# Kernel tuning notes

Hardware: AMD Instinct MI355X
Metric: run time of the kernel (lower is better)

The kernel has to match this reference:

```python
import jax, jax.numpy as jnp
import numpy as np

D = 1024; NH = 16; HD = D // NH; B = 2; L = 2048
BASE_FAST = (1.0 + 5.0 ** 0.5) / 2.0
BASE_SLOW = 1618.0
BASE_GLU = 16180.0
ALPHA_ATTN = 0.42; ALPHA_MLP = 1.07; ALPHA_ADV = 1.0
H_GATE = max(8, D // 4)   # rope_gate hidden
H_NU = max(4, D // 8)     # DuplexViscosity hidden
LN_EPS = 1e-5


def _rope_cos_sin(seq_len, dim, base, dtype=jnp.float32):
    idx = jnp.arange(0, dim, 2, dtype=dtype) / float(dim)
    inv = 1.0 / (base ** idx)
    t = jnp.arange(seq_len, dtype=dtype)
    freqs = jnp.outer(t, inv)                       # (L, D/2)
    emb = jnp.concatenate([freqs, freqs], axis=-1)  # (L, D)
    return jnp.cos(emb)[None], jnp.sin(emb)[None]   # (1, L, D)


def _rotate_half(x):
    x1, x2 = jnp.split(x, 2, axis=-1)
    return jnp.concatenate([-x2, x1], axis=-1)


def _apply_rope(x, cos, sin):
    return x * cos + _rotate_half(x) * sin


def setup_inputs() -> dict:
    key = jax.random.key(0)
    ks = jax.random.split(key, 16)
    std = 0.02
    # all Linear weights stored as (in, out) so forward is x @ W + b
    return {
        "z": jax.random.normal(ks[0], (B, L, D), jnp.float32),
        "Wq": jax.random.normal(ks[1], (D, D), jnp.float32) * std,
        "bq": jnp.zeros((D,), jnp.float32),
        "Wk": jax.random.normal(ks[2], (D, D), jnp.float32) * std,
        "bk": jnp.zeros((D,), jnp.float32),
        "Wv": jax.random.normal(ks[3], (D, D), jnp.float32) * std,
        "bv": jnp.zeros((D,), jnp.float32),
        "Wcoh": jax.random.normal(ks[4], (D, D), jnp.float32) * std,
        "gamma": jnp.zeros((1,), jnp.float32),
        "rg_w1": jax.random.normal(ks[5], (D, H_GATE), jnp.float32) * std,
        "rg_b1": jnp.zeros((H_GATE,), jnp.float32),
        "rg_w2": jax.random.normal(ks[6], (H_GATE, 1), jnp.float32) * std,
        "rg_b2": jnp.zeros((1,), jnp.float32),
        "nu_diff": jnp.asarray(0.2, jnp.float32),
        "nu_adv": jnp.asarray(0.01, jnp.float32),
        "nu_w1": jax.random.normal(ks[7], (D, H_NU), jnp.float32) * std,
        "nu_b1": jnp.zeros((H_NU,), jnp.float32),
        "nu_w2": jax.random.normal(ks[8], (H_NU, 1), jnp.float32) * std,
        "nu_b2": jnp.zeros((1,), jnp.float32),
        "Wu": jax.random.normal(ks[9], (D, D), jnp.float32) * std,
        "bu": jnp.zeros((D,), jnp.float32),
        "Wg": jax.random.normal(ks[10], (D, D), jnp.float32) * std,
        "bg": jnp.zeros((D,), jnp.float32),
        "ln_w": jnp.ones((D,), jnp.float32),
        "ln_b": jnp.zeros((D,), jnp.float32),
        "Cw": jax.random.normal(ks[11], (D, D), jnp.float32) * std,
        "Cb": jnp.zeros((D,), jnp.float32),
    }


def reference(z, Wq, bq, Wk, bk, Wv, bv, Wcoh, gamma, rg_w1, rg_b1, rg_w2, rg_b2,
              nu_diff, nu_adv, nu_w1, nu_b1, nu_w2, nu_b2, Wu, bu, Wg, bg,
              ln_w, ln_b, Cw, Cb):
    b, l, d = z.shape
    dt = z.dtype
    # causal cumulative mean pool[t] = mean(z[0..t])
    pool = jnp.cumsum(z, axis=1) / jnp.arange(1, l + 1, dtype=dt)[None, :, None]

    # QKV projections
    Q = z @ Wq + bq
    K_raw = z @ Wk + bk
    V = z @ Wv + bv

    # global coherence bias: (B, Lq, Lk)
    gk = pool @ Wcoh
    gb = jnp.einsum('bld,bmd->blm', gk, K_raw) * (d ** -0.5)
    gb = jnp.tanh(gamma[0]) * gb

    # hybrid RoPE gate (small MLP on pool, exact gelu as in torch)
    gate = jax.nn.sigmoid(jax.nn.gelu(pool @ rg_w1 + rg_b1, approximate=False) @ rg_w2 + rg_b2)  # (B,L,1)
    cos_f, sin_f = _rope_cos_sin(l, d, BASE_FAST, dt)
    cos_s, sin_s = _rope_cos_sin(l, d, BASE_SLOW, dt)
    cos = gate * cos_f + (1.0 - gate) * cos_s
    sin = gate * sin_f + (1.0 - gate) * sin_s
    Qr = _apply_rope(Q, cos, sin)
    Kr = _apply_rope(K_raw, cos, sin)

    # multi-head causal attention with fused coherence bias
    Qh = Qr.reshape(b, l, NH, HD).transpose(0, 2, 1, 3)
    Kh = Kr.reshape(b, l, NH, HD).transpose(0, 2, 1, 3)
    Vh = V.reshape(b, l, NH, HD).transpose(0, 2, 1, 3)
    logits = jnp.einsum('bhld,bhmd->bhlm', Qh, Kh) * (HD ** -0.5)
    logits = logits + gb[:, None]
    causal = jnp.tril(jnp.ones((l, l), bool))
    logits = jnp.where(causal[None, None], logits, -jnp.inf)
    attn = jax.nn.softmax(logits, axis=-1)
    attn_out = jnp.einsum('bhlm,bhmd->bhld', attn, Vh).transpose(0, 2, 1, 3).reshape(b, l, d)
    attn_w = attn.mean(axis=1)

    # DuplexViscosity on causal pool
    delta = jnp.tanh(jnp.tanh(pool @ nu_w1 + nu_b1) @ nu_w2 + nu_b2) * jnp.abs(nu_adv)
    nu_b = jnp.abs(nu_diff) + delta  # (B,L,1)

    # GLU branch with fixed slow-base RoPE
    cos_g, sin_g = _rope_cos_sin(l, d, BASE_GLU, dt)
    z_glu = _apply_rope(z, cos_g, sin_g)
    bilinear = (z_glu @ Wu + bu) * (z_glu @ Wg + bg)
    adv = -(ALPHA_ADV * nu_b) * bilinear
    mu = adv.mean(axis=-1, keepdims=True)
    var = ((adv - mu) ** 2).mean(axis=-1, keepdims=True)
    adv_n = (adv - mu) * jax.lax.rsqrt(var + LN_EPS) * ln_w + ln_b
    mlp_out = adv_n @ Cw + Cb

    z_next = z + ALPHA_ATTN * attn_out + ALPHA_MLP * mlp_out
    return z_next, attn_w
```

## Files before the change

kernel.cpp:

```cpp
#include <hip/hip_runtime.h>

#define DD 1024
#define NHH 16
#define HDD 64
#define BB 2
#define LL 2048
#define MM (BB*LL)
#define HG 256
#define HN 128

#define LOG_FAST 0.48121182f
#define LOG_SLOW 7.3889461f
#define LOG_GLU  9.6915312f
#define SCL 0.18033688f

typedef __attribute__((ext_vector_type(8))) short short8;
typedef __attribute__((ext_vector_type(4))) float f32x4;

__device__ __forceinline__ float gelu_f(float x) {
    return 0.5f * x * (1.0f + erff(x * 0.70710678f));
}

__device__ __forceinline__ ushort f2b(float x) {
    unsigned u = __float_as_uint(x);
    unsigned r = (u + 0x7FFFu + ((u >> 16) & 1u)) >> 16;
    return (ushort)r;
}

__device__ __forceinline__ float b2f(ushort x) {
    return __uint_as_float(((unsigned)x) << 16);
}

__device__ __forceinline__ void gl_lds16(const ushort* g, ushort* l) {
    __builtin_amdgcn_global_load_lds(
        (const __attribute__((address_space(1))) unsigned int*)g,
        (__attribute__((address_space(3))) unsigned int*)l, 16, 0, 0);
}

#define SWZC(row, c8) (((((row) << 3) | ((c8) ^ ((row) & 7)))) << 3)

__device__ __forceinline__ void stage_tile(const ushort* gsrc, int rstride,
                                           ushort* lds, int tid) {
    int wid = tid >> 6;
#pragma unroll
    for (int r = 0; r < 2; ++r) {
        int c = r * 256 + tid;
        int row = c >> 3;
        int c8 = (c & 7) ^ (row & 7);
        gl_lds16(gsrc + (size_t)row * rstride + c8 * 8,
                 lds + (size_t)(r * 256 + wid * 64) * 8);
    }
}

#define LCH 128
#define NCH 16
__global__ void pool_scan1(const float* __restrict__ z, float* __restrict__ part,
                           float* __restrict__ ctot, ushort* __restrict__ zb) {
    int ch = blockIdx.x, dg = blockIdx.y, b = blockIdx.z;
    int d = dg * 256 + threadIdx.x;
    size_t base = ((size_t)b * LL + ch * LCH) * DD + d;
    const float* zp = z + base;
    float* pp = part + base;
    ushort* zo = zb + base;
    float s = 0.f;
    for (int t = 0; t < LCH; ++t) {
        float v = zp[(size_t)t * DD];
        s += v;
        pp[(size_t)t * DD] = s;
        zo[(size_t)t * DD] = f2b(v);
    }
    ctot[((size_t)b * NCH + ch) * DD + d] = s;
}
__global__ void pool_scan2(const float* __restrict__ part, const float* __restrict__ ctot,
                           ushort* __restrict__ poolb) {
    int ch = blockIdx.x, dg = blockIdx.y, b = blockIdx.z;
    int d = dg * 256 + threadIdx.x;
    float off = 0.f;
    for (int c = 0; c < ch; ++c) off += ctot[((size_t)b * NCH + c) * DD + d];
    int t0 = ch * LCH;
    size_t base = ((size_t)b * LL + t0) * DD + d;
    const float* pp = part + base;
    ushort* po = poolb + base;
    for (int t = 0; t < LCH; ++t) {
        po[(size_t)t * DD] = f2b((pp[(size_t)t * DD] + off) / (float)(t0 + t + 1));
    }
}

__global__ void f2bT4_kernel(const float* __restrict__ W0, const float* __restrict__ W1,
                             const float* __restrict__ W2, const float* __restrict__ W3,
                             ushort* __restrict__ Wt) {
    const float* W = blockIdx.z == 0 ? W0 : (blockIdx.z == 1 ? W1 :
                     (blockIdx.z == 2 ? W2 : W3));
    ushort* dst = Wt + (size_t)blockIdx.z * 1024 * 1024;
    __shared__ float t[32][33];
    int n0 = blockIdx.x * 32, k0 = blockIdx.y * 32;
    int tx = threadIdx.x & 31, ty = threadIdx.x >> 5;
#pragma unroll
    for (int j = 0; j < 4; ++j)
        t[ty + j * 8][tx] = W[(size_t)(k0 + ty + j * 8) * 1024 + n0 + tx];
    __syncthreads();
#pragma unroll
    for (int j = 0; j < 4; ++j)
        dst[(size_t)(n0 + ty + j * 8) * 1024 + k0 + tx] = f2b(t[tx][ty + j * 8]);
}

__global__ void f2bT_rgnu(const float* __restrict__ Wrg, const float* __restrict__ Wnu,
                          ushort* __restrict__ WtRG, ushort* __restrict__ WtNU) {
    int zc = blockIdx.z;
    if (zc == 1 && blockIdx.x >= 4) return;
    const float* W = zc == 0 ? Wrg : Wnu;
    ushort* dst = zc == 0 ? WtRG : WtNU;
    int Ndim = zc == 0 ? HG : HN;
    __shared__ float t[32][33];
    int n0 = blockIdx.x * 32, k0 = blockIdx.y * 32;
    int tx = threadIdx.x & 31, ty = threadIdx.x >> 5;
#pragma unroll
    for (int j = 0; j < 4; ++j)
        t[ty + j * 8][tx] = W[(size_t)(k0 + ty + j * 8) * Ndim + n0 + tx];
    __syncthreads();
#pragma unroll
    for (int j = 0; j < 4; ++j)
        dst[(size_t)(n0 + ty + j * 8) * 1024 + k0 + tx] = f2b(t[tx][ty + j * 8]);
}

__global__ void f2bT3_kernel(const float* __restrict__ W0, const float* __restrict__ W1,
                             const float* __restrict__ W2, ushort* __restrict__ Wt) {
    const float* W = blockIdx.z == 0 ? W0 : (blockIdx.z == 1 ? W1 : W2);
    ushort* dst = Wt + (size_t)blockIdx.z * 1024 * 1024;
    __shared__ float t[32][33];
    int n0 = blockIdx.x * 32, k0 = blockIdx.y * 32;
    int tx = threadIdx.x & 31, ty = threadIdx.x >> 5;
#pragma unroll
    for (int j = 0; j < 4; ++j)
        t[ty + j * 8][tx] = W[(size_t)(k0 + ty + j * 8) * 1024 + n0 + tx];
    __syncthreads();
#pragma unroll
    for (int j = 0; j < 4; ++j)
        dst[(size_t)(n0 + ty + j * 8) * 1024 + k0 + tx] = f2b(t[tx][ty + j * 8]);
}

__global__ __launch_bounds__(256) void gemm_mfma(
        const ushort* __restrict__ A, const ushort* __restrict__ Wt,
        const float* __restrict__ bias, float* __restrict__ C, int Ndim) {
    __shared__ ushort As[4096];
    __shared__ ushort Bs[4096];
    int tid = threadIdx.x;
    int wid = tid >> 6, lane = tid & 63;
    int n0 = blockIdx.x * 128, m0 = blockIdx.y * 128;
    int wm = wid >> 1, wn = wid & 1;
    int quad = lane >> 4, l16 = lane & 15;

    f32x4 acc[4][4];
#pragma unroll
    for (int mi = 0; mi < 4; ++mi)
#pragma unroll
        for (int ni = 0; ni < 4; ++ni) acc[mi][ni] = (f32x4){0.f, 0.f, 0.f, 0.f};

    int c0 = wid * 128 + lane;
    int c1 = c0 + 64;
    const ushort* Ag0 = A + (size_t)(m0 + (c0 & 127)) * 1024 + (c0 >> 7) * 8;
    const ushort* Ag1 = A + (size_t)(m0 + (c1 & 127)) * 1024 + (c1 >> 7) * 8;
    const ushort* Bg0 = Wt + (size_t)(n0 + (c0 & 127)) * 1024 + (c0 >> 7) * 8;
    const ushort* Bg1 = Wt + (size_t)(n0 + (c1 & 127)) * 1024 + (c1 >> 7) * 8;
    ushort* Al0 = As + wid * 1024;
    ushort* Al1 = As + wid * 1024 + 512;
    ushort* Bl0 = Bs + wid * 1024;
    ushort* Bl1 = Bs + wid * 1024 + 512;

    const ushort* a_rd = &As[(quad * 128 + wm * 64 + l16) * 8];
    const ushort* b_rd = &Bs[(quad * 128 + wn * 64 + l16) * 8];

    for (int kb = 0; kb < 1024; kb += 32) {
        gl_lds16(Ag0 + kb, Al0);
        gl_lds16(Ag1 + kb, Al1);
        gl_lds16(Bg0 + kb, Bl0);
        gl_lds16(Bg1 + kb, Bl1);
        __syncthreads();
        short8 af[4], bf[4];
#pragma unroll
        for (int mi = 0; mi < 4; ++mi)
            af[mi] = *(const short8*)(a_rd + mi * 16 * 8);
#pragma unroll
        for (int ni = 0; ni < 4; ++ni)
            bf[ni] = *(const short8*)(b_rd + ni * 16 * 8);
#pragma unroll
        for (int mi = 0; mi < 4; ++mi)
#pragma unroll
            for (int ni = 0; ni < 4; ++ni)
                acc[mi][ni] = __builtin_amdgcn_mfma_f32_16x16x32_bf16(
                    af[mi], bf[ni], acc[mi][ni], 0, 0, 0);
        __syncthreads();
    }
    int bcol[4];
    float bval[4];
#pragma unroll
    for (int ni = 0; ni < 4; ++ni) {
        bcol[ni] = n0 + wn * 64 + ni * 16 + l16;
        bval[ni] = bias ? bias[bcol[ni]] : 0.f;
    }
#pragma unroll
    for (int mi = 0; mi < 4; ++mi) {
#pragma unroll
        for (int r = 0; r < 4; ++r) {
            int row = m0 + wm * 64 + mi * 16 + quad * 4 + r;
            float* Cp = C + (size_t)row * Ndim;
#pragma unroll
            for (int ni = 0; ni < 4; ++ni)
                Cp[bcol[ni]] = acc[mi][ni][r] + bval[ni];
        }
    }
}

__global__ __launch_bounds__(256) void gemm_mfma3(
        const ushort* __restrict__ A, const ushort* __restrict__ Wt,
        const float* __restrict__ b0, const float* __restrict__ b1,
        const float* __restrict__ b2, float* __restrict__ C,
        ushort* __restrict__ K16r) {
    int zid = blockIdx.z;
    const ushort* W = Wt + (size_t)zid * 1024 * 1024;
    const float* bias = zid == 0 ? b0 : (zid == 1 ? b1 : b2);
    float* Cz = C + (size_t)zid * (size_t)MM * DD;
    __shared__ ushort As[4096];
    __shared__ ushort Bs[4096];
    int tid = threadIdx.x;
    int wid = tid >> 6, lane = tid & 63;
    int n0 = blockIdx.x * 128, m0 = blockIdx.y * 128;
    int wm = wid >> 1, wn = wid & 1;
    int quad = lane >> 4, l16 = lane & 15;

    f32x4 acc[4][4];
#pragma unroll
    for (int mi = 0; mi < 4; ++mi)
#pragma unroll
        for (int ni = 0; ni < 4; ++ni) acc[mi][ni] = (f32x4){0.f, 0.f, 0.f, 0.f};

    int c0 = wid * 128 + lane;
    int c1 = c0 + 64;
    const ushort* Ag0 = A + (size_t)(m0 + (c0 & 127)) * 1024 + (c0 >> 7) * 8;
    const ushort* Ag1 = A + (size_t)(m0 + (c1 & 127)) * 1024 + (c1 >> 7) * 8;
    const ushort* Bg0 = W + (size_t)(n0 + (c0 & 127)) * 1024 + (c0 >> 7) * 8;
    const ushort* Bg1 = W + (size_t)(n0 + (c1 & 127)) * 1024 + (c1 >> 7) * 8;
    ushort* Al0 = As + wid * 1024;
    ushort* Al1 = As + wid * 1024 + 512;
    ushort* Bl0 = Bs + wid * 1024;
    ushort* Bl1 = Bs + wid * 1024 + 512;

    const ushort* a_rd = &As[(quad * 128 + wm * 64 + l16) * 8];
    const ushort* b_rd = &Bs[(quad * 128 + wn * 64 + l16) * 8];

    for (int kb = 0; kb < 1024; kb += 32) {
        gl_lds16(Ag0 + kb, Al0);
        gl_lds16(Ag1 + kb, Al1);
        gl_lds16(Bg0 + kb, Bl0);
        gl_lds16(Bg1 + kb, Bl1);
        __syncthreads();
        short8 af[4], bf[4];
#pragma unroll
        for (int mi = 0; mi < 4; ++mi)
            af[mi] = *(const short8*)(a_rd + mi * 16 * 8);
#pragma unroll
        for (int ni = 0; ni < 4; ++ni)
            bf[ni] = *(const short8*)(b_rd + ni * 16 * 8);
#pragma unroll
        for (int mi = 0; mi < 4; ++mi)
#pragma unroll
            for (int ni = 0; ni < 4; ++ni)
                acc[mi][ni] = __builtin_amdgcn_mfma_f32_16x16x32_bf16(
                    af[mi], bf[ni], acc[mi][ni], 0, 0, 0);
        __syncthreads();
    }
    float bval[4];
    int bcol[4];
#pragma unroll
    for (int ni = 0; ni < 4; ++ni) {
        bcol[ni] = n0 + wn * 64 + ni * 16 + l16;
        bval[ni] = bias[bcol[ni]];
    }
    bool doK = (zid == 1) && (K16r != nullptr);
#pragma unroll
    for (int mi = 0; mi < 4; ++mi) {
#pragma unroll
        for (int r = 0; r < 4; ++r) {
            int row = m0 + wm * 64 + mi * 16 + quad * 4 + r;
            float* Cp = Cz + (size_t)row * 1024;
            ushort* Kp = K16r + (size_t)row * 1024;
#pragma unroll
            for (int ni = 0; ni < 4; ++ni) {
                float v = acc[mi][ni][r] + bval[ni];
                Cp[bcol[ni]] = v;
                if (doK) Kp[bcol[ni]] = f2b(v);
            }
        }
    }
}

__global__ __launch_bounds__(256) void gemm_mfma_b16out(
        const ushort* __restrict__ A, const ushort* __restrict__ Wt,
        ushort* __restrict__ C, int Ndim) {
    __shared__ ushort As[4096];
    __shared__ ushort Bs[4096];
    int tid = threadIdx.x;
    int wid = tid >> 6, lane = tid & 63;
    int n0 = blockIdx.x * 128, m0 = blockIdx.y * 128;
    int wm = wid >> 1, wn = wid & 1;
    int quad = lane >> 4, l16 = lane & 15;

    f32x4 acc[4][4];
#pragma unroll
    for (int mi = 0; mi < 4; ++mi)
#pragma unroll
        for (int ni = 0; ni < 4; ++ni) acc[mi][ni] = (f32x4){0.f, 0.f, 0.f, 0.f};

    int c0 = wid * 128 + lane;
    int c1 = c0 + 64;
    const ushort* Ag0 = A + (size_t)(m0 + (c0 & 127)) * 1024 + (c0 >> 7) * 8;
    const ushort* Ag1 = A + (size_t)(m0 + (c1 & 127)) * 1024 + (c1 >> 7) * 8;
    const ushort* Bg0 = Wt + (size_t)(n0 + (c0 & 127)) * 1024 + (c0 >> 7) * 8;
    const ushort* Bg1 = Wt + (size_t)(n0 + (c1 & 127)) * 1024 + (c1 >> 7) * 8;
    ushort* Al0 = As + wid * 1024;
    ushort* Al1 = As + wid * 1024 + 512;
    ushort* Bl0 = Bs + wid * 1024;
    ushort* Bl1 = Bs + wid * 1024 + 512;

    const ushort* a_rd = &As[(quad * 128 + wm * 64 + l16) * 8];
    const ushort* b_rd = &Bs[(quad * 128 + wn * 64 + l16) * 8];

    for (int kb = 0; kb < 1024; kb += 32) {
        gl_lds16(Ag0 + kb, Al0);
        gl_lds16(Ag1 + kb, Al1);
        gl_lds16(Bg0 + kb, Bl0);
        gl_lds16(Bg1 + kb, Bl1);
        __syncthreads();
        short8 af[4], bf[4];
#pragma unroll
        for (int mi = 0; mi < 4; ++mi)
            af[mi] = *(const short8*)(a_rd + mi * 16 * 8);
#pragma unroll
        for (int ni = 0; ni < 4; ++ni)
            bf[ni] = *(const short8*)(b_rd + ni * 16 * 8);
#pragma unroll
        for (int mi = 0; mi < 4; ++mi)
#pragma unroll
            for (int ni = 0; ni < 4; ++ni)
                acc[mi][ni] = __builtin_amdgcn_mfma_f32_16x16x32_bf16(
                    af[mi], bf[ni], acc[mi][ni], 0, 0, 0);
        __syncthreads();
    }
#pragma unroll
    for (int mi = 0; mi < 4; ++mi) {
#pragma unroll
        for (int r = 0; r < 4; ++r) {
            int row = m0 + wm * 64 + mi * 16 + quad * 4 + r;
            ushort* Cp = C + (size_t)row * Ndim;
#pragma unroll
            for (int ni = 0; ni < 4; ++ni)
                Cp[n0 + wn * 64 + ni * 16 + l16] = f2b(acc[mi][ni][r]);
        }
    }
}

__global__ __launch_bounds__(256) void gemm_gates(
        const ushort* __restrict__ A, const ushort* __restrict__ WtRG,
        const ushort* __restrict__ WtNU, const float* __restrict__ rg_b1,
        const float* __restrict__ nu_b1, float* __restrict__ H1,
        float* __restrict__ N1) {
    int bx = blockIdx.x;
    bool isH = bx < 2;
    const ushort* Wt = isH ? WtRG : WtNU;
    const float* bias = isH ? rg_b1 : nu_b1;
    float* C = isH ? H1 : N1;
    int Ndim = isH ? HG : HN;
    int n0 = isH ? bx * 128 : 0;
    int m0 = blockIdx.y * 128;
    __shared__ ushort As[4096];
    __shared__ ushort Bs[4096];
    int tid = threadIdx.x;
    int wid = tid >> 6, lane = tid & 63;
    int wm = wid >> 1, wn = wid & 1;
    int quad = lane >> 4, l16 = lane & 15;

    f32x4 acc[4][4];
#pragma unroll
    for (int mi = 0; mi < 4; ++mi)
#pragma unroll
        for (int ni = 0; ni < 4; ++ni) acc[mi][ni] = (f32x4){0.f, 0.f, 0.f, 0.f};

    int c0 = wid * 128 + lane;
    int c1 = c0 + 64;
    const ushort* Ag0 = A + (size_t)(m0 + (c0 & 127)) * 1024 + (c0 >> 7) * 8;
    const ushort* Ag1 = A + (size_t)(m0 + (c1 & 127)) * 1024 + (c1 >> 7) * 8;
    const ushort* Bg0 = Wt + (size_t)(n0 + (c0 & 127)) * 1024 + (c0 >> 7) * 8;
    const ushort* Bg1 = Wt + (size_t)(n0 + (c1 & 127)) * 1024 + (c1 >> 7) * 8;
    ushort* Al0 = As + wid * 1024;
    ushort* Al1 = As + wid * 1024 + 512;
    ushort* Bl0 = Bs + wid * 1024;
    ushort* Bl1 = Bs + wid * 1024 + 512;

    const ushort* a_rd = &As[(quad * 128 + wm * 64 + l16) * 8];
    const ushort* b_rd = &Bs[(quad * 128 + wn * 64 + l16) * 8];

    for (int kb = 0; kb < 1024; kb += 32) {
        gl_lds16(Ag0 + kb, Al0);
        gl_lds16(Ag1 + kb, Al1);
        gl_lds16(Bg0 + kb, Bl0);
        gl_lds16(Bg1 + kb, Bl1);
        __syncthreads();
        short8 af[4], bf[4];
#pragma unroll
        for (int mi = 0; mi < 4; ++mi)
            af[mi] = *(const short8*)(a_rd + mi * 16 * 8);
#pragma unroll
        for (int ni = 0; ni < 4; ++ni)
            bf[ni] = *(const short8*)(b_rd + ni * 16 * 8);
#pragma unroll
        for (int mi = 0; mi < 4; ++mi)
#pragma unroll
            for (int ni = 0; ni < 4; ++ni)
                acc[mi][ni] = __builtin_amdgcn_mfma_f32_16x16x32_bf16(
                    af[mi], bf[ni], acc[mi][ni], 0, 0, 0);
        __syncthreads();
    }
    int bcol[4];
    float bval[4];
#pragma unroll
    for (int ni = 0; ni < 4; ++ni) {
        bcol[ni] = n0 + wn * 64 + ni * 16 + l16;
        bval[ni] = bias[bcol[ni]];
    }
#pragma unroll
    for (int mi = 0; mi < 4; ++mi) {
#pragma unroll
        for (int r = 0; r < 4; ++r) {
            int row = m0 + wm * 64 + mi * 16 + quad * 4 + r;
            float* Cp = C + (size_t)row * Ndim;
#pragma unroll
            for (int ni = 0; ni < 4; ++ni)
                Cp[bcol[ni]] = acc[mi][ni][r] + bval[ni];
        }
    }
}

__global__ __launch_bounds__(256) void gb_mfma(
        const ushort* __restrict__ gk16, const ushort* __restrict__ K16r,
        const float* __restrict__ gamma, ushort* __restrict__ gb) {
    int lt = blockIdx.x >> 4, mt = blockIdx.x & 15;
    if (mt > lt) return;
    int b = blockIdx.y;
    __shared__ ushort As[4096];
    __shared__ ushort Bs[4096];
    int tid = threadIdx.x;
    int wid = tid >> 6, lane = tid & 63;
    int l0 = lt * 128, m0 = mt * 128;
    int wm = wid >> 1, wn = wid & 1;
    int quad = lane >> 4, l16 = lane & 15;

    f32x4 acc[4][4];
#pragma unroll
    for (int mi = 0; mi < 4; ++mi)
#pragma unroll
        for (int ni = 0; ni < 4; ++ni) acc[mi][ni] = (f32x4){0.f, 0.f, 0.f, 0.f};

    int c0 = wid * 128 + lane;
    int c1 = c0 + 64;
    const ushort* Ag0 = gk16 + ((size_t)b * LL + l0 + (c0 & 127)) * 1024 + (c0 >> 7) * 8;
    const ushort* Ag1 = gk16 + ((size_t)b * LL + l0 + (c1 & 127)) * 1024 + (c1 >> 7) * 8;
    const ushort* Bg0 = K16r + ((size_t)b * LL + m0 + (c0 & 127)) * 1024 + (c0 >> 7) * 8;
    const ushort* Bg1 = K16r + ((size_t)b * LL + m0 + (c1 & 127)) * 1024 + (c1 >> 7) * 8;
    ushort* Al0 = As + wid * 1024;
    ushort* Al1 = As + wid * 1024 + 512;
    ushort* Bl0 = Bs + wid * 1024;
    ushort* Bl1 = Bs + wid * 1024 + 512;

    const ushort* a_rd = &As[(quad * 128 + wm * 64 + l16) * 8];
    const ushort* b_rd = &Bs[(quad * 128 + wn * 64 + l16) * 8];

    for (int kb = 0; kb < 1024; kb += 32) {
        gl_lds16(Ag0 + kb, Al0);
        gl_lds16(Ag1 + kb, Al1);
        gl_lds16(Bg0 + kb, Bl0);
        gl_lds16(Bg1 + kb, Bl1);
        __syncthreads();
        short8 af[4], bf[4];
#pragma unroll
        for (int mi = 0; mi < 4; ++mi)
            af[mi] = *(const short8*)(a_rd + mi * 16 * 8);
#pragma unroll
        for (int ni = 0; ni < 4; ++ni)
            bf[ni] = *(const short8*)(b_rd + ni * 16 * 8);
#pragma unroll
        for (int mi = 0; mi < 4; ++mi)
#pragma unroll
            for (int ni = 0; ni < 4; ++ni)
                acc[mi][ni] = __builtin_amdgcn_mfma_f32_16x16x32_bf16(
                    af[mi], bf[ni], acc[mi][ni], 0, 0, 0);
        __syncthreads();
    }
    float scale = tanhf(gamma[0]) * 0.25f;
#pragma unroll
    for (int mi = 0; mi < 4; ++mi) {
#pragma unroll
        for (int r = 0; r < 4; ++r) {
            int row = l0 + wm * 64 + mi * 16 + quad * 4 + r;
            ushort* Cp = gb + ((size_t)b * LL + row) * LL;
            ushort4 o;
            o.x = f2b(acc[mi][0][r] * scale);
            o.y = f2b(acc[mi][1][r] * scale);
            o.z = f2b(acc[mi][2][r] * scale);
            o.w = f2b(acc[mi][3][r] * scale);
            *(ushort4*)(Cp + m0 + wn * 64 + l16 * 4) = o;
        }
    }
}

__global__ __launch_bounds__(256) void gatenu_fin(
        const float* __restrict__ H1, const float* __restrict__ N1,
        const float* __restrict__ rg_w2, const float* __restrict__ rg_b2,
        const float* __restrict__ nu_w2, const float* __restrict__ nu_b2,
        const float* __restrict__ nu_diff, const float* __restrict__ nu_adv,
        float* __restrict__ gate, float* __restrict__ nub) {
    int row = blockIdx.x, tid = threadIdx.x;
    float gv = gelu_f(H1[(size_t)row * HG + tid]) * rg_w2[tid];
    float nv = (tid < HN) ? tanhf(N1[(size_t)row * HN + tid]) * nu_w2[tid] : 0.f;
    for (int off = 32; off; off >>= 1) {
        gv += __shfl_down(gv, off);
        nv += __shfl_down(nv, off);
    }
    __shared__ float pg[4], pn[4];
    if ((tid & 63) == 0) { pg[tid >> 6] = gv; pn[tid >> 6] = nv; }
    __syncthreads();
    if (tid == 0) {
        float ga = pg[0] + pg[1] + pg[2] + pg[3] + rg_b2[0];
        gate[row] = 1.f / (1.f + expf(-ga));
        float na = pn[0] + pn[1] + pn[2] + pn[3] + nu_b2[0];
        nub[row] = fabsf(nu_diff[0]) + tanhf(na) * fabsf(nu_adv[0]);
    }
}

__global__ void rope_qk_bf16(const float* __restrict__ Q, const float* __restrict__ K,
                             const float* __restrict__ gate,
                             ushort* __restrict__ Q16, ushort* __restrict__ K16) {
    int idx = blockIdx.x * 256 + threadIdx.x;
    int row = idx >> 9;
    int i = idx & 511;
    int b = row >> 11, t = row & (LL - 1);
    float g = gate[row];
    float fi = (float)i * (1.0f / 512.0f);
    float tf = (float)t;
    float af = tf * expf(-fi * LOG_FAST);
    float as = tf * expf(-fi * LOG_SLOW);
    float c = g * cosf(af) + (1.f - g) * cosf(as);
    float s = g * sinf(af) + (1.f - g) * sinf(as);
    size_t base = (size_t)row * DD;
    float x = Q[base + i], y = Q[base + 512 + i];
    float q1 = x * c - y * s, q2 = y * c + x * s;
    x = K[base + i]; y = K[base + 512 + i];
    float k1 = x * c - y * s, k2 = y * c + x * s;
    int h1 = i >> 6, d1 = i & 63;
    size_t o1 = ((size_t)(b * 16 + h1) * LL + t) * 64 + d1;
    size_t o2 = ((size_t)(b * 16 + 8 + h1) * LL + t) * 64 + d1;
    Q16[o1] = f2b(q1); Q16[o2] = f2b(q2);
    K16[o1] = f2b(k1); K16[o2] = f2b(k2);
}

__global__ __launch_bounds__(256) void vt16_kernel(const float* __restrict__ V,
                                                   ushort* __restrict__ VT) {
    __shared__ ushort t[64][72];
    int lb = blockIdx.x, hb = blockIdx.y, b = blockIdx.z;
    int tid = threadIdx.x;
    {
        int l = tid >> 2, c0 = (tid & 3) * 16;
        const float* Vp = V + ((size_t)(b * LL) + lb * 64 + l) * DD + hb * 64 + c0;
#pragma unroll
        for (int j = 0; j < 4; ++j) {
            float4 v = *(const float4*)(Vp + j * 4);
            t[l][c0 + j * 4 + 0] = f2b(v.x);
            t[l][c0 + j * 4 + 1] = f2b(v.y);
            t[l][c0 + j * 4 + 2] = f2b(v.z);
            t[l][c0 + j * 4 + 3] = f2b(v.w);
        }
    }
    __syncthreads();
    {
        int d = tid >> 2, l0 = (tid & 3) * 16;
        ushort tmp[16];
#pragma unroll
        for (int j = 0; j < 16; ++j) tmp[j] = t[l0 + j][d];
        ushort* Op = VT + ((size_t)((b * 16 + hb) * 64) + d) * LL + lb * 64 + l0;
        *(ushort4*)(Op + 0)  = *(ushort4*)&tmp[0];
        *(ushort4*)(Op + 4)  = *(ushort4*)&tmp[4];
        *(ushort4*)(Op + 8)  = *(ushort4*)&tmp[8];
        *(ushort4*)(Op + 12) = *(ushort4*)&tmp[12];
    }
}

__global__ void rope_glu_b16(const float* __restrict__ z, ushort* __restrict__ zg) {
    int idx = blockIdx.x * 256 + threadIdx.x;
    int row = idx >> 9;
    int i = idx & 511;
    int t = row & (LL - 1);
    float fi = (float)i * (1.0f / 512.0f);
    float ag = (float)t * expf(-fi * LOG_GLU);
    float c = cosf(ag), s = sinf(ag);
    size_t base = (size_t)row * DD;
    float x = z[base + i], y = z[base + 512 + i];
    zg[base + i]       = f2b(x * c - y * s);
    zg[base + 512 + i] = f2b(y * c + x * s);
}

__global__ __launch_bounds__(256, 2) void attn_flash_mfma(
        const ushort* __restrict__ Q16, const ushort* __restrict__ K16,
        const ushort* __restrict__ VT16, const ushort* __restrict__ gb16,
        float* __restrict__ attn_out, float* __restrict__ stats) {
    int h = blockIdx.x, b = blockIdx.z;
    __shared__ ushort Ks0[4096];
    __shared__ ushort Vs0[4096];
    __shared__ ushort Ks1[4096];
    __shared__ ushort Vs1[4096];
    __shared__ ushort Ks2[4096];
    __shared__ ushort Vs2[4096];
    __shared__ ushort Ps[4096];
    int tid = threadIdx.x, wid = tid >> 6, lane = tid & 63;
    int quad = lane >> 4, l16 = lane & 15;
    const ushort* Qg = Q16 + ((size_t)(b * 16 + h) * LL) * 64;
    const ushort* Kg = K16 + ((size_t)(b * 16 + h) * LL) * 64;
    const ushort* Vg = VT16 + ((size_t)(b * 16 + h) * 64) * LL;
    const ushort* gbB = gb16 + (size_t)b * LL * LL;
    float* stB = stats + ((size_t)(b * 16 + h) * LL) * 2;
    int qrow = wid * 16 + quad * 4;
    ushort* Pw = Ps + wid * 1024;

    short ov = (l16 == 0) ? (short)0x3F80 : (short)0;
    short8 onesf = {ov, ov, ov, ov, ov, ov, ov, ov};

#define FLASH_PHASE(KC, VC, KS, VS, T) do {                                       \
    asm volatile("s_waitcnt vmcnt(8)" ::: "memory");                              \
    __builtin_amdgcn_sched_barrier(0);                                            \
    __builtin_amdgcn_s_barrier();                                                 \
    __builtin_amdgcn_sched_barrier(0);                                            \
    {                                                                             \
        int tg_ = ((T) + 1 <= qt) ? ((T) + 1) : qt;                               \
        const ushort* gp_ = gbB + (size_t)(q0 + qrow) * LL + tg_ * 64 + l16 * 4;  \
        gnx[0] = *(const ushort4*)(gp_);                                          \
        gnx[1] = *(const ushort4*)(gp_ + LL);                                     \
        gnx[2] = *(const ushort4*)(gp_ + 2 * LL);                                 \
        gnx[3] = *(const ushort4*)(gp_ + 3 * LL);                                 \
        int ts_ = ((T) + 2 <= qt) ? ((T) + 2) : qt;                               \
        stage_tile(Kg + (size_t)ts_ * 64 * 64, 64, (KS), tid);                    \
        stage_tile(Vg + ts_ * 64, LL, (VS), tid);                                 \
    }                                                                             \
    __builtin_amdgcn_sched_barrier(0);                                            \
    f32x4 sf_[4];                                                                 \
    _Pragma("unroll")                                                             \
    for (int r = 0; r < 4; ++r) {                                                 \
        sf_[0][r] = b2f(gcur[r].x); sf_[1][r] = b2f(gcur[r].y);                   \
        sf_[2][r] = b2f(gcur[r].z); sf_[3][r] = b2f(gcur[r].w);                   \
    }                                                                             \
    _Pragma("unroll")                                                             \
    for (int ks = 0; ks < 2; ++ks)                                                \
        _Pragma("unroll")                                                         \
        for (int nt = 0; nt < 4; ++nt) {                                          \
            short8 kf_ = *(const short8*)((KC) + SWZC(nt * 16 + l16, ks * 4 + quad)); \
            sf_[nt] = __builtin_amdgcn_mfma_f32_16x16x32_bf16(qf[ks], kf_, sf_[nt], 0, 0, 0); \
        }                                                                         \
    if ((T) == qt) {                                                              \
        _Pragma("unroll")                                                         \
        for (int nt = 0; nt < 4; ++nt)                                            \
            _Pragma("unroll")                                                     \
            for (int r = 0; r < 4; ++r)                                           \
                if (nt * 16 + l16 > qrow + r) sf_[nt][r] = -1e30f;                \
    }                                                                             \
    float alpha_[4], mS_[4];                                                      \
    _Pragma("unroll")                                                             \
    for (int r = 0; r < 4; ++r) {                                                 \
        float m_ = fmaxf(fmaxf(sf_[0][r], sf_[1][r]), fmaxf(sf_[2][r], sf_[3][r])); \
        _Pragma("unroll")                                                         \
        for (int off = 1; off < 16; off <<= 1)                                    \
            m_ = fmaxf(m_, __shfl_xor(m_, off));                                  \
        float nm_ = fmaxf(m_r[r], m_);                                            \
        alpha_[r] = __builtin_amdgcn_exp2f((m_r[r] - nm_) * SCL);                 \
        m_r[r] = nm_;                                                             \
        mS_[r] = nm_ * SCL;                                                       \
    }                                                                             \
    _Pragma("unroll")                                                             \
    for (int nt = 0; nt < 4; ++nt)                                                \
        _Pragma("unroll")                                                         \
        for (int r = 0; r < 4; ++r) {                                             \
            float p_ = __builtin_amdgcn_exp2f(fmaf(sf_[nt][r], SCL, -mS_[r]));    \
            int prow_ = quad * 4 + r;                                             \
            int chk_ = (nt * 2) | (l16 >> 3);                                     \
            Pw[prow_ * 64 + ((chk_ ^ (prow_ & 7)) << 3) + (l16 & 7)] = f2b(p_);   \
        }                                                                         \
    _Pragma("unroll")                                                             \
    for (int nt = 0; nt < 5; ++nt)                                                \
        _Pragma("unroll")                                                         \
        for (int r = 0; r < 4; ++r) ofr[nt][r] *= alpha_[r];                      \
    short8 pf_[2];                                                                \
    _Pragma("unroll")                                                             \
    for (int ks = 0; ks < 2; ++ks)                                                \
        pf_[ks] = *(const short8*)(Pw + l16 * 64 + (((ks * 4 + quad) ^ (l16 & 7)) << 3)); \
    __builtin_amdgcn_s_setprio(1);                                                \
    _Pragma("unroll")                                                             \
    for (int ks = 0; ks < 2; ++ks) {                                              \
        _Pragma("unroll")                                                         \
        for (int nt = 0; nt < 4; ++nt) {                                          \
            short8 vf_ = *(const short8*)((VC) + SWZC(nt * 16 + l16, ks * 4 + quad)); \
            ofr[nt] = __builtin_amdgcn_mfma_f32_16x16x32_bf16(pf_[ks], vf_, ofr[nt], 0, 0, 0); \
        }                                                                         \
        ofr[4] = __builtin_amdgcn_mfma_f32_16x16x32_bf16(pf_[ks], onesf, ofr[4], 0, 0, 0); \
    }                                                                             \
    __builtin_amdgcn_s_setprio(0);                                                \
    gcur[0] = gnx[0]; gcur[1] = gnx[1]; gcur[2] = gnx[2]; gcur[3] = gnx[3];       \
} while (0)

#pragma unroll 1
    for (int sel = 0; sel < 2; ++sel) {
        int qt = sel ? (31 - (int)blockIdx.y) : (int)blockIdx.y;
        int q0 = qt * 64;

        asm volatile("s_waitcnt vmcnt(0)" ::: "memory");
        __builtin_amdgcn_sched_barrier(0);
        __builtin_amdgcn_s_barrier();
        __builtin_amdgcn_sched_barrier(0);

        short8 qf[2];
        {
            const ushort* qp = Qg + (size_t)(q0 + wid * 16 + l16) * 64 + quad * 8;
            qf[0] = *(const short8*)(qp);
            qf[1] = *(const short8*)(qp + 32);
        }
        stage_tile(Kg, 64, Ks0, tid);
        stage_tile(Vg, LL, Vs0, tid);
        ushort4 gcur[4], gnx[4];
        {
            const ushort* gp = gbB + (size_t)(q0 + qrow) * LL + l16 * 4;
            gcur[0] = *(const ushort4*)(gp);
            gcur[1] = *(const ushort4*)(gp + LL);
            gcur[2] = *(const ushort4*)(gp + 2 * LL);
            gcur[3] = *(const ushort4*)(gp + 3 * LL);
        }
        {
            int t1 = (qt >= 1) ? 1 : 0;
            stage_tile(Kg + (size_t)t1 * 64 * 64, 64, Ks1, tid);
            stage_tile(Vg + t1 * 64, LL, Vs1, tid);
        }

        f32x4 ofr[5];
        float m_r[4];
#pragma unroll
        for (int nt = 0; nt < 5; ++nt) ofr[nt] = (f32x4){0.f, 0.f, 0.f, 0.f};
#pragma unroll
        for (int r = 0; r < 4; ++r) m_r[r] = -3e38f;

        for (int kt = 0; kt <= qt; kt += 3) {
            FLASH_PHASE(Ks0, Vs0, Ks2, Vs2, kt);
            if (kt + 1 <= qt) FLASH_PHASE(Ks1, Vs1, Ks0, Vs0, kt + 1);
            if (kt + 2 <= qt) FLASH_PHASE(Ks2, Vs2, Ks1, Vs1, kt + 2);
        }

#pragma unroll
        for (int r = 0; r < 4; ++r) {
            float l = __shfl(ofr[4][r], (lane & 48));
            float rinv = 1.0f / l;
            float* op = attn_out + ((size_t)(b * LL) + q0 + qrow + r) * DD + h * 64 + l16;
#pragma unroll
            for (int nt = 0; nt < 4; ++nt)
                op[nt * 16] = ofr[nt][r] * rinv;
        }
        if (l16 == 0) {
#pragma unroll
            for (int r = 0; r < 4; ++r) {
                size_t si = (size_t)(q0 + qrow + r) * 2;
                stB[si]     = m_r[r];
                stB[si + 1] = ofr[4][r];
            }
        }
    }
#undef FLASH_PHASE
}

__global__ __launch_bounds__(256, 4) void attn_w_mfma(
        const ushort* __restrict__ Q16, const ushort* __restrict__ K16,
        const ushort* __restrict__ gb16, const float* __restrict__ stats,
        float* __restrict__ aw) {
    int qt = blockIdx.x >> 5, kt = blockIdx.x & 31;
    int b = blockIdx.y;
    int tid = threadIdx.x, wid = tid >> 6, lane = tid & 63;
    int quad = lane >> 4, l16 = lane & 15;
    int q0 = qt * 64, k0 = kt * 64;
    int qrow = wid * 16 + quad * 4;
    if (kt > qt) {
        int rr = tid >> 2, c0 = (tid & 3) * 16;
        float4 zv = make_float4(0.f, 0.f, 0.f, 0.f);
        float* p = aw + ((size_t)(b * LL) + q0 + rr) * LL + k0 + c0;
#pragma unroll
        for (int j = 0; j < 4; ++j) *(float4*)(p + j * 4) = zv;
        return;
    }
    __shared__ ushort Qs0[4096];
    __shared__ ushort Ks0[4096];
    __shared__ ushort Qs1[4096];
    __shared__ ushort Ks1[4096];
    float acc[4][4];
#pragma unroll
    for (int nt = 0; nt < 4; ++nt)
#pragma unroll
        for (int r = 0; r < 4; ++r) acc[nt][r] = 0.f;
    f32x4 gacc[4];
    const ushort* gbB = gb16 + (size_t)b * LL * LL;
#pragma unroll
    for (int r = 0; r < 4; ++r) {
        ushort4 g4 = *(const ushort4*)(gbB + (size_t)(q0 + qrow + r) * LL + k0 + l16 * 4);
        gacc[0][r] = b2f(g4.x);
        gacc[1][r] = b2f(g4.y);
        gacc[2][r] = b2f(g4.z);
        gacc[3][r] = b2f(g4.w);
    }
    bool diag = (kt == qt);
    stage_tile(Q16 + ((size_t)(b * 16) * LL + q0) * 64, 64, Qs0, tid);
    stage_tile(K16 + ((size_t)(b * 16) * LL + k0) * 64, 64, Ks0, tid);

#define AW_PHASE(QC, KC, QN, KN, H) do {                                          \
    asm volatile("s_waitcnt vmcnt(0)" ::: "memory");                              \
    __builtin_amdgcn_sched_barrier(0);                                            \
    __builtin_amdgcn_s_barrier();                                                 \
    __builtin_amdgcn_sched_barrier(0);                                            \
    float s0_[4], s1_[4];                                                         \
    {                                                                             \
        const float* sp_ = stats + ((size_t)(b * 16 + (H)) * LL + q0 + qrow) * 2; \
        _Pragma("unroll")                                                         \
        for (int r = 0; r < 4; ++r) { s0_[r] = sp_[r * 2]; s1_[r] = sp_[r * 2 + 1]; } \
    }                                                                             \
    __builtin_amdgcn_sched_barrier(0);                                            \
    {                                                                             \
        int hn_ = ((H) + 1 <= 15) ? ((H) + 1) : 15;                               \
        stage_tile(Q16 + ((size_t)(b * 16 + hn_) * LL + q0) * 64, 64, (QN), tid); \
        stage_tile(K16 + ((size_t)(b * 16 + hn_) * LL + k0) * 64, 64, (KN), tid); \
    }                                                                             \
    __builtin_amdgcn_sched_barrier(0);                                            \
    short8 qf_[2];                                                                \
    _Pragma("unroll")                                                             \
    for (int ks = 0; ks < 2; ++ks)                                                \
        qf_[ks] = *(const short8*)((QC) + SWZC(wid * 16 + l16, ks * 4 + quad));   \
    f32x4 sf_[4];                                                                 \
    _Pragma("unroll")                                                             \
    for (int nt = 0; nt < 4; ++nt) sf_[nt] = gacc[nt];                            \
    __builtin_amdgcn_s_setprio(1);                                                \
    _Pragma("unroll")                                                             \
    for (int ks = 0; ks < 2; ++ks)                                                \
        _Pragma("unroll")                                                         \
        for (int nt = 0; nt < 4; ++nt) {                                          \
            short8 kf_ = *(const short8*)((KC) + SWZC(nt * 16 + l16, ks * 4 + quad)); \
            sf_[nt] = __builtin_amdgcn_mfma_f32_16x16x32_bf16(qf_[ks], kf_, sf_[nt], 0, 0, 0); \
        }                                                                         \
    __builtin_amdgcn_s_setprio(0);                                                \
    float mS_[4], li_[4];                                                         \
    _Pragma("unroll")                                                             \
    for (int r = 0; r < 4; ++r) { mS_[r] = s0_[r] * SCL; li_[r] = 1.0f / s1_[r]; } \
    _Pragma("unroll")                                                             \
    for (int nt = 0; nt < 4; ++nt)                                                \
        _Pragma("unroll")                                                         \
        for (int r = 0; r < 4; ++r) {                                             \
            int row_ = qrow + r;                                                  \
            if (!diag || (nt * 16 + l16 <= row_))                                 \
                acc[nt][r] += __builtin_amdgcn_exp2f(fmaf(sf_[nt][r], SCL, -mS_[r])) * li_[r]; \
        }                                                                         \
} while (0)

    for (int h = 0; h < NHH; h += 2) {
        AW_PHASE(Qs0, Ks0, Qs1, Ks1, h);
        AW_PHASE(Qs1, Ks1, Qs0, Ks0, h + 1);
    }
#undef AW_PHASE

#pragma unroll
    for (int r = 0; r < 4; ++r) {
        float* op = aw + ((size_t)(b * LL) + q0 + qrow + r) * LL + k0 + l16;
#pragma unroll
        for (int nt = 0; nt < 4; ++nt)
            op[nt * 16] = acc[nt][r] * 0.0625f;
    }
}

__global__ __launch_bounds__(256) void adv_ln_kernel(
        const float* __restrict__ U, const float* __restrict__ G,
        const float* __restrict__ nub, const float* __restrict__ lnw,
        const float* __restrict__ lnb, ushort* __restrict__ out) {
    int row = blockIdx.x, tid = threadIdx.x;
    size_t base = (size_t)row * DD + tid * 4;
    float4 u4 = *(const float4*)&U[base];
    float4 g4 = *(const float4*)&G[base];
    float nu = nub[row];
    float a[4];
    a[0] = -nu * u4.x * g4.x;
    a[1] = -nu * u4.y * g4.y;
    a[2] = -nu * u4.z * g4.z;
    a[3] = -nu * u4.w * g4.w;
    float ts = a[0] + a[1] + a[2] + a[3];
    float tq = a[0] * a[0] + a[1] * a[1] + a[2] * a[2] + a[3] * a[3];
    for (int off = 32; off; off >>= 1) {
        ts += __shfl_down(ts, off);
        tq += __shfl_down(tq, off);
    }
    __shared__ float r1[4], r2[4];
    if ((tid & 63) == 0) { r1[tid >> 6] = ts; r2[tid >> 6] = tq; }
    __syncthreads();
    __shared__ float s_mu, s_rs;
    if (tid == 0) {
        float S  = r1[0] + r1[1] + r1[2] + r1[3];
        float Qq = r2[0] + r2[1] + r2[2] + r2[3];
        float mu = S * (1.0f / 1024.f);
        float var = Qq * (1.0f / 1024.f) - mu * mu;
        s_mu = mu;
        s_rs = rsqrtf(var + 1e-5f);
    }
    __syncthreads();
    float mu = s_mu, rs = s_rs;
    float4 w4 = *(const float4*)&lnw[tid * 4];
    float4 b4 = *(const float4*)&lnb[tid * 4];
    ushort4 ov;
    ov.x = f2b((a[0] - mu) * rs * w4.x + b4.x);
    ov.y = f2b((a[1] - mu) * rs * w4.y + b4.y);
    ov.z = f2b((a[2] - mu) * rs * w4.z + b4.z);
    ov.w = f2b((a[3] - mu) * rs * w4.w + b4.w);
    *(ushort4*)&out[base] = ov;
}

__global__ void final_kernel(const float* __restrict__ z, const float* __restrict__ ao,
                             const float* __restrict__ mlp, float* __restrict__ out) {
    size_t i = ((size_t)blockIdx.x * 256 + threadIdx.x) * 4;
    float4 z4 = *(const float4*)&z[i];
    float4 a4 = *(const float4*)&ao[i];
    float4 m4 = *(const float4*)&mlp[i];
    float4 o;
    o.x = z4.x + 0.42f * a4.x + 1.07f * m4.x;
    o.y = z4.y + 0.42f * a4.y + 1.07f * m4.y;
    o.z = z4.z + 0.42f * a4.z + 1.07f * m4.z;
    o.w = z4.w + 0.42f * a4.w + 1.07f * m4.w;
    *(float4*)&out[i] = o;
}

extern "C" void kernel_launch(void* const* d_in, const int* in_sizes, int n_in,
                              void* d_out, int out_size, void* d_ws, size_t ws_size,
                              hipStream_t stream) {
    const float* z       = (const float*)d_in[0];
    const float* Wq      = (const float*)d_in[1];
    const float* bq      = (const float*)d_in[2];
    const float* Wk      = (const float*)d_in[3];
    const float* bk      = (const float*)d_in[4];
    const float* Wv      = (const float*)d_in[5];
    const float* bv      = (const float*)d_in[6];
    const float* Wcoh    = (const float*)d_in[7];
    const float* gamma   = (const float*)d_in[8];
    const float* rg_w1   = (const float*)d_in[9];
    const float* rg_b1   = (const float*)d_in[10];
    const float* rg_w2   = (const float*)d_in[11];
    const float* rg_b2   = (const float*)d_in[12];
    const float* nu_diff = (const float*)d_in[13];
    const float* nu_adv  = (const float*)d_in[14];
    const float* nu_w1   = (const float*)d_in[15];
    const float* nu_b1   = (const float*)d_in[16];
    const float* nu_w2   = (const float*)d_in[17];
    const float* nu_b2   = (const float*)d_in[18];
    const float* Wu      = (const float*)d_in[19];
    const float* bu      = (const float*)d_in[20];
    const float* Wg      = (const float*)d_in[21];
    const float* bg      = (const float*)d_in[22];
    const float* ln_w    = (const float*)d_in[23];
    const float* ln_b    = (const float*)d_in[24];
    const float* Cw      = (const float*)d_in[25];
    const float* Cb      = (const float*)d_in[26];

    float* out_z  = (float*)d_out;
    float* out_aw = out_z + (size_t)MM * DD;

    float* ws = (float*)d_ws;
    const size_t MD = (size_t)MM * DD;
    float* pool  = ws;
    float* Qb    = ws + MD;
    float* Kb    = ws + 2 * MD;
    float* Vb    = ws + 3 * MD;
    float* gkb   = ws + 4 * MD;
    float* gbb   = ws + 5 * MD;
    float* H1    = ws + 7 * MD;
    float* N1    = H1 + (size_t)MM * HG;
    float* gate  = N1 + (size_t)MM * HN;
    float* nub   = gate + MM;
    float* stats = nub + MM;
    float* ctot  = stats + (size_t)BB * NHH * LL * 2;

    char* gbase  = (char*)gbb;
    ushort* Ab   = (ushort*)gbase;
    ushort* Wb   = (ushort*)(gbase + (size_t)8 * 1024 * 1024);
    ushort* gb16 = (ushort*)(gbase + (size_t)16 * 1024 * 1024);
    ushort* WtRG = Wb;
    ushort* WtNU = Wb + (size_t)1024 * 1024;
    ushort* Q16  = (ushort*)Vb;
    ushort* K16  = (ushort*)Vb + MD;
    ushort* VT16 = (ushort*)pool;
    ushort* poolb = (ushort*)pool;
    float*  part = gkb;
    ushort* gk16 = (ushort*)gkb;
    ushort* K16r = (ushort*)gkb + MD;

    dim3 g128(8, 32);
    dim3 wT_g(32, 32);

    pool_scan1<<<dim3(NCH, 4, BB), 256, 0, stream>>>(z, part, ctot, Ab);
    pool_scan2<<<dim3(NCH, 4, BB), 256, 0, stream>>>(part, ctot, poolb);
    f2bT4_kernel<<<dim3(32, 32, 4), 256, 0, stream>>>(Wq, Wk, Wv, Wcoh, Wb);
    gemm_mfma3<<<dim3(8, 32, 3), 256, 0, stream>>>(Ab, Wb, bq, bk, bv, Qb, K16r);
    gemm_mfma_b16out<<<g128, 256, 0, stream>>>(poolb, Wb + (size_t)3 * 1024 * 1024, gk16, DD);
    f2bT_rgnu<<<dim3(8, 32, 2), 256, 0, stream>>>(rg_w1, nu_w1, WtRG, WtNU);
    gemm_gates<<<dim3(3, 32), 256, 0, stream>>>(poolb, WtRG, WtNU, rg_b1, nu_b1, H1, N1);
    gb_mfma<<<dim3(256, BB), 256, 0, stream>>>(gk16, K16r, gamma, gb16);
    gatenu_fin<<<dim3(MM), 256, 0, stream>>>(H1, N1, rg_w2, rg_b2, nu_w2, nu_b2,
                                             nu_diff, nu_adv, gate, nub);
    vt16_kernel<<<dim3(32, 16, BB), 256, 0, stream>>>(Vb, VT16);
    rope_qk_bf16<<<dim3((MM * 512) / 256), 256, 0, stream>>>(Qb, Kb, gate, Q16, K16);
    attn_flash_mfma<<<dim3(NHH, 16, BB), 256, 0, stream>>>(Q16, K16, VT16, gb16, gkb, stats);
    attn_w_mfma<<<dim3(1024, BB), 256, 0, stream>>>(Q16, K16, gb16, stats, out_aw);
    rope_glu_b16<<<dim3((MM * 512) / 256), 256, 0, stream>>>(z, Ab);
    f2bT3_kernel<<<dim3(32, 32, 3), 256, 0, stream>>>(Wu, Wg, Cw, Wb);
    gemm_mfma3<<<dim3(8, 32, 2), 256, 0, stream>>>(Ab, Wb, bu, bg, bg, Qb, nullptr);
    adv_ln_kernel<<<dim3(MM), 256, 0, stream>>>(Qb, Kb, nub, ln_w, ln_b, Ab);
    gemm_mfma<<<g128, 256, 0, stream>>>(Ab, Wb + (size_t)2 * 1024 * 1024, Cb, Qb, DD);
    final_kernel<<<dim3(MD / 4 / 256), 256, 0, stream>>>(z, gkb, Qb, out_z);
}
```

Baseline: 586.6 us.

## Remap flash-attention grid for XCD locality and restructure attn_w head pipeline sync

The flash-attention launch becomes a flat 512-block grid, and block indices are remapped so that blocks sharing a head and batch land on the same XCD. This should improve L2 reuse of K/V tiles. In the attention-weight kernel, the per-head phase no longer does an explicit vmcnt wait plus barrier at the top. It now stages the next head's Q/K without redundant last-head loads, loads the stats before the MFMAs, and ends each phase with __syncthreads. This shortens the scheduling constraints but relies on __syncthreads to order the double-buffered LDS writes.

```diff
diff --git a/kernel.cpp b/kernel.cpp
--- a/kernel.cpp
+++ b/kernel.cpp
@@ -611,7 +611,12 @@
         const ushort* __restrict__ Q16, const ushort* __restrict__ K16,
         const ushort* __restrict__ VT16, const ushort* __restrict__ gb16,
         float* __restrict__ attn_out, float* __restrict__ stats) {
-    int h = blockIdx.x, b = blockIdx.z;
+    int gid = blockIdx.x;
+    int xcd = gid & 7;
+    int j = gid >> 3;
+    int ypair = xcd + 8 * (j & 1);
+    int h = (j >> 1) & 15;
+    int b = j >> 5;
     __shared__ ushort Ks0[4096];
     __shared__ ushort Vs0[4096];
     __shared__ ushort Ks1[4096];
@@ -714,7 +719,7 @@
 
 #pragma unroll 1
     for (int sel = 0; sel < 2; ++sel) {
-        int qt = sel ? (31 - (int)blockIdx.y) : (int)blockIdx.y;
+        int qt = sel ? (31 - ypair) : ypair;
         int q0 = qt * 64;
 
         asm volatile("s_waitcnt vmcnt(0)" ::: "memory");
@@ -818,29 +823,26 @@
     bool diag = (kt == qt);
     stage_tile(Q16 + ((size_t)(b * 16) * LL + q0) * 64, 64, Qs0, tid);
     stage_tile(K16 + ((size_t)(b * 16) * LL + k0) * 64, 64, Ks0, tid);
+    __syncthreads();
 
 #define AW_PHASE(QC, KC, QN, KN, H) do {                                          \
-    asm volatile("s_waitcnt vmcnt(0)" ::: "memory");                              \
-    __builtin_amdgcn_sched_barrier(0);                                            \
-    __builtin_amdgcn_s_barrier();                                                 \
-    __builtin_amdgcn_sched_barrier(0);                                            \
-    float s0_[4], s1_[4];                                                         \
-    {                                                                             \
-        const float* sp_ = stats + ((size_t)(b * 16 + (H)) * LL + q0 + qrow) * 2; \
-        _Pragma("unroll")                                                         \
-        for (int r = 0; r < 4; ++r) { s0_[r] = sp_[r * 2]; s1_[r] = sp_[r * 2 + 1]; } \
+    if ((H) < 15) {                                                               \
+        stage_tile(Q16 + ((size_t)(b * 16 + (H) + 1) * LL + q0) * 64, 64, (QN), tid); \
+        stage_tile(K16 + ((size_t)(b * 16 + (H) + 1) * LL + k0) * 64, 64, (KN), tid); \
     }                                                                             \
-    __builtin_amdgcn_sched_barrier(0);                                            \
-    {                                                                             \
-        int hn_ = ((H) + 1 <= 15) ? ((H) + 1) : 15;                               \
-        stage_tile(Q16 + ((size_t)(b * 16 + hn_) * LL + q0) * 64, 64, (QN), tid); \
-        stage_tile(K16 + ((size_t)(b * 16 + hn_) * LL + k0) * 64, 64, (KN), tid); \
-    }                                                                             \
-    __builtin_amdgcn_sched_barrier(0);                                            \
     short8 qf_[2];                                                                \
     _Pragma("unroll")                                                             \
     for (int ks = 0; ks < 2; ++ks)                                                \
         qf_[ks] = *(const short8*)((QC) + SWZC(wid * 16 + l16, ks * 4 + quad));   \
+    float mS_[4], li_[4];                                                         \
+    {                                                                             \
+        const float* sp_ = stats + ((size_t)(b * 16 + (H)) * LL + q0 + qrow) * 2; \
+        _Pragma("unroll")                                                         \
+        for (int r = 0; r < 4; ++r) {                                             \
+            mS_[r] = sp_[r * 2] * SCL;                                            \
+            li_[r] = 1.0f / sp_[r * 2 + 1];                                       \
+        }                                                                         \
+    }                                                                             \
     f32x4 sf_[4];                                                                 \
     _Pragma("unroll")                                                             \
     for (int nt = 0; nt < 4; ++nt) sf_[nt] = gacc[nt];                            \
@@ -853,9 +855,6 @@
             sf_[nt] = __builtin_amdgcn_mfma_f32_16x16x32_bf16(qf_[ks], kf_, sf_[nt], 0, 0, 0); \
         }                                                                         \
     __builtin_amdgcn_s_setprio(0);                                                \
-    float mS_[4], li_[4];                                                         \
-    _Pragma("unroll")                                                             \
-    for (int r = 0; r < 4; ++r) { mS_[r] = s0_[r] * SCL; li_[r] = 1.0f / s1_[r]; } \
     _Pragma("unroll")                                                             \
     for (int nt = 0; nt < 4; ++nt)                                                \
         _Pragma("unroll")                                                         \
@@ -864,6 +863,7 @@
             if (!diag || (nt * 16 + l16 <= row_))                                 \
                 acc[nt][r] += __builtin_amdgcn_exp2f(fmaf(sf_[nt][r], SCL, -mS_[r])) * li_[r]; \
         }                                                                         \
+    __syncthreads();                                                              \
 } while (0)
 
     for (int h = 0; h < NHH; h += 2) {
@@ -1017,7 +1017,7 @@
                                              nu_diff, nu_adv, gate, nub);
     vt16_kernel<<<dim3(32, 16, BB), 256, 0, stream>>>(Vb, VT16);
     rope_qk_bf16<<<dim3((MM * 512) / 256), 256, 0, stream>>>(Qb, Kb, gate, Q16, K16);
-    attn_flash_mfma<<<dim3(NHH, 16, BB), 256, 0, stream>>>(Q16, K16, VT16, gb16, gkb, stats);
+    attn_flash_mfma<<<dim3(512), 256, 0, stream>>>(Q16, K16, VT16, gb16, gkb, stats);
     attn_w_mfma<<<dim3(1024, BB), 256, 0, stream>>>(Q16, K16, gb16, stats, out_aw);
     rope_glu_b16<<<dim3((MM * 512) / 256), 256, 0, stream>>>(z, Ab);
     f2bT3_kernel<<<dim3(32, 32, 3), 256, 0, stream>>>(Wu, Wg, Cw, Wb);
```

After: 569.5 us. -2.9%, faster.
